# Optimization experiments

Hardware: AMD Instinct MI355X
Metric: run time of the kernel (lower is better)

Reference implementation:

```python
import jax, jax.numpy as jnp
import numpy as np

LOGISTIC_R = 3.8
COUPLING_ITERS = 5


def _linear_interp(v, L):
    """PyTorch F.interpolate(mode='linear', align_corners=False) along last axis.
    v: [..., K] real -> [..., L] real."""
    K = v.shape[-1]
    pos = (jnp.arange(L, dtype=jnp.float32) + 0.5) * (K / L) - 0.5
    pos = jnp.clip(pos, 0.0, K - 1)  # torch clamps src coords into range
    i0 = jnp.floor(pos).astype(jnp.int32)
    i1 = jnp.minimum(i0 + 1, K - 1)
    w = pos - i0
    return v[..., i0] * (1.0 - w) + v[..., i1] * w


def setup_inputs() -> dict:
    key = jax.random.key(0)
    ks = jax.random.split(key, 4)
    B, Cin, Cout, L, K = 16, 64, 64, 8192, 64
    return {
        "x_real": jax.random.normal(ks[0], (B, Cin, L), jnp.float32),
        "x_imag": jax.random.normal(ks[1], (B, Cin, L), jnp.float32),
        "kernel_real": jax.random.normal(ks[2], (Cout, Cin, K), jnp.float32),
        "kernel_imag": jax.random.normal(ks[3], (Cout, Cin, K), jnp.float32),
        "alpha_D": jnp.ones((1,), jnp.float32),
    }


def reference(x_real, x_imag, kernel_real, kernel_imag, alpha_D):
    x = x_real + 1j * x_imag  # [B, Cin, L] complex64
    L = x.shape[-1]

    # --- logistic self-coupling on magnitude (per-batch min/max over (C, L)) ---
    mag = jnp.abs(x)
    phase = jnp.angle(x)
    mmin = mag.min(axis=(-1, -2), keepdims=True)
    mmax = mag.max(axis=(-1, -2), keepdims=True)
    xn = (mag - mmin) / (mmax - mmin + 1e-10)
    for _ in range(COUPLING_ITERS):
        xn = LOGISTIC_R * xn * (1.0 - xn)
    mag_c = xn * (mmax - mmin) + mmin
    x_coupled = mag_c * jnp.exp(1j * phase)

    # --- spectral conv: FFT, per-pair kernel interpolation, complex MAC ---
    x_fft = jnp.fft.fft(x_coupled, axis=-1)  # [B, Cin, L]
    kfft = jnp.fft.fft(kernel_real + 1j * kernel_imag, axis=-1)  # [O, I, K]
    kmag = _linear_interp(jnp.abs(kfft), L)    # [O, I, L]
    kph = _linear_interp(jnp.angle(kfft), L)   # [O, I, L]
    kint = kmag * jnp.exp(1j * kph)            # [O, I, L] complex64
    out_fft = jnp.einsum('bjl,ijl->bil', x_fft, kint)  # replaces O*I python loop
    out = jnp.fft.ifft(out_fft, axis=-1)  # [B, O, L]

    # --- optical probe activation: sin(omega*0 + phi0 + alpha_D * lambda) ---
    theta = alpha_D[0] * jnp.arange(L, dtype=jnp.float32)
    act = jnp.sin(theta)  # omega*t = 0, phi0 = 0
    return out * act
```

## Files before the change

### kernel.cpp

```cpp
#include <hip/hip_runtime.h>
#include <hip/hip_fp16.h>
#include <hip/hip_bf16.h>
#include <math.h>

#define L 8192
#define LOG2L 13
#define B 16
#define CIN 64
#define COUT 64
#define KK 64

#define PI_F 3.14159265358979323846f

typedef float f4v __attribute__((ext_vector_type(4)));
typedef short s8v __attribute__((ext_vector_type(8)));

__device__ __forceinline__ int PHI(int n) { return n ^ ((((n >> 5) ^ (n >> 9)) & 15) << 1); }

__device__ __forceinline__ void nsincos(float ang, float* sn, float* cs) {
    float r = ang * 0.15915494309189535f;
    r = r - floorf(r);
    *sn = __builtin_amdgcn_sinf(r);
    *cs = __builtin_amdgcn_cosf(r);
}

__device__ __forceinline__ unsigned short f2bf(float f) {
    unsigned u = __builtin_bit_cast(unsigned, f);
    u += 0x7FFFu + ((u >> 16) & 1u);
    return (unsigned short)(u >> 16);
}
__device__ __forceinline__ unsigned pkbf(float a, float b) {
    unsigned ua = __builtin_bit_cast(unsigned, a) + 0x8000u;
    unsigned ub = __builtin_bit_cast(unsigned, b) + 0x8000u;
    return (ub & 0xFFFF0000u) | (ua >> 16);
}

template<int INV>
__device__ __forceinline__ void bfly4(float& u0r, float& u0i, float& u1r, float& u1i,
                                      float& v0r, float& v0i, float& v1r, float& v1i,
                                      float w1r, float w1i, float w2r, float w2i) {
    float A0r = u0r + v0r, A0i = u0i + v0i;
    float t0r = u0r - v0r, t0i = u0i - v0i;
    float B0r = t0r * w1r - t0i * w1i, B0i = t0r * w1i + t0i * w1r;
    float A1r = u1r + v1r, A1i = u1i + v1i;
    float t1r = u1r - v1r, t1i = u1i - v1i;
    float wr = t1r * w1r - t1i * w1i, wi = t1r * w1i + t1i * w1r;
    float B1r = INV ? -wi : wi;
    float B1i = INV ? wr : -wr;
    u0r = A0r + A1r; u0i = A0i + A1i;
    float d0r = A0r - A1r, d0i = A0i - A1i;
    u1r = d0r * w2r - d0i * w2i; u1i = d0r * w2i + d0i * w2r;
    v0r = B0r + B1r; v0i = B0i + B1i;
    float d1r = B0r - B1r, d1i = B0i - B1i;
    v1r = d1r * w2r - d1i * w2i; v1i = d1r * w2i + d1i * w2r;
}

template<int INV>
__device__ __forceinline__ void radix16(float* xr, float* xi, float wc, float ws) {
    const float C8 = 0.9238795325112867f, S8 = 0.3826834323650898f, C4 = 0.7071067811865476f;
    float e1r = C8, e1i = INV ? S8 : -S8;
    float e2r = C4, e2i = INV ? C4 : -C4;
    float e3r = S8, e3i = INV ? C8 : -C8;
    float a1r[4], a1i[4], a2r[4], a2i[4];
    a1r[0] = wc;                    a1i[0] = ws;
    a1r[1] = wc * e1r - ws * e1i;   a1i[1] = wc * e1i + ws * e1r;
    a1r[2] = wc * e2r - ws * e2i;   a1i[2] = wc * e2i + ws * e2r;
    a1r[3] = wc * e3r - ws * e3i;   a1i[3] = wc * e3i + ws * e3r;
#pragma unroll
    for (int q = 0; q < 4; ++q) {
        a2r[q] = a1r[q] * a1r[q] - a1i[q] * a1i[q];
        a2i[q] = 2.f * a1r[q] * a1i[q];
    }
    float b1r = a2r[0] * a2r[0] - a2i[0] * a2i[0], b1i = 2.f * a2r[0] * a2i[0];
    float b2r = b1r * b1r - b1i * b1i, b2i = 2.f * b1r * b1i;
#pragma unroll
    for (int q = 0; q < 4; ++q)
        bfly4<INV>(xr[q], xi[q], xr[q + 4], xi[q + 4], xr[q + 8], xi[q + 8],
                   xr[q + 12], xi[q + 12], a1r[q], a1i[q], a2r[q], a2i[q]);
#pragma unroll
    for (int c = 0; c < 4; ++c)
        bfly4<INV>(xr[4 * c], xi[4 * c], xr[4 * c + 1], xi[4 * c + 1],
                   xr[4 * c + 2], xi[4 * c + 2], xr[4 * c + 3], xi[4 * c + 3],
                   b1r, b1i, b2r, b2i);
}

__global__ __launch_bounds__(256) void k_reduce1(const float* __restrict__ xr,
                                                 const float* __restrict__ xi,
                                                 float* __restrict__ pmin,
                                                 float* __restrict__ pmax) {
    int bid = blockIdx.x;
    int batch = bid >> 6, slice = bid & 63;
    size_t base = (size_t)batch * CIN * L + (size_t)slice * L;
    int tid = threadIdx.x;
    float mn = 3.4e38f, mx = 0.0f;
    for (int r = 0; r < 32; ++r) {
        int idx = r * 256 + tid;
        float a = xr[base + idx], b = xi[base + idx];
        float m = sqrtf(a * a + b * b);
        mn = fminf(mn, m);
        mx = fmaxf(mx, m);
    }
    __shared__ float smn[4], smx[4];
    for (int off = 32; off >= 1; off >>= 1) {
        mn = fminf(mn, __shfl_down(mn, off));
        mx = fmaxf(mx, __shfl_down(mx, off));
    }
    int wave = tid >> 6;
    if ((tid & 63) == 0) { smn[wave] = mn; smx[wave] = mx; }
    __syncthreads();
    if (tid == 0) {
        for (int w = 1; w < 4; ++w) { mn = fminf(mn, smn[w]); mx = fmaxf(mx, smx[w]); }
        pmin[bid] = mn;
        pmax[bid] = mx;
    }
}

__global__ __launch_bounds__(64) void k_reduce2(const float* __restrict__ pmin,
                                                const float* __restrict__ pmax,
                                                float* __restrict__ mmin,
                                                float* __restrict__ mmax) {
    int b = blockIdx.x, t = threadIdx.x;
    float mn = pmin[b * 64 + t], mx = pmax[b * 64 + t];
    for (int off = 32; off >= 1; off >>= 1) {
        mn = fminf(mn, __shfl_down(mn, off));
        mx = fmaxf(mx, __shfl_down(mx, off));
    }
    if (t == 0) { mmin[b] = mn; mmax[b] = mx; }
}

__global__ __launch_bounds__(64) void k_kstats(const float* __restrict__ kr,
                                               const float* __restrict__ ki,
                                               float* __restrict__ Pmag,
                                               float* __restrict__ Pph) {
    int row = blockIdx.x;
    int k = threadIdx.x;
    __shared__ float sr[64], si[64];
    sr[k] = kr[row * 64 + k];
    si[k] = ki[row * 64 + k];
    __syncthreads();
    float ar = 0.f, ai = 0.f;
    for (int n = 0; n < 64; ++n) {
        int m = (n * k) & 63;
        float ang = -2.0f * PI_F * (float)m * (1.0f / 64.0f);
        float s, c;
        __sincosf(ang, &s, &c);
        ar += sr[n] * c - si[n] * s;
        ai += sr[n] * s + si[n] * c;
    }
    float mag = sqrtf(ar * ar + ai * ai);
    float ph = atan2f(ai, ar);
    int io = row >> 6, jn = row & 63;
    int ic = io >> 4, l15 = io & 15;
    int jc = jn >> 5, hi = (jn >> 3) & 3, e = jn & 7;
    int lane = hi * 16 + l15;
    size_t off = (size_t)k * 4096 + (ic * 2 + jc) * 512 + lane * 8 + e;
    Pmag[off] = mag;
    Pph[off] = ph;
    if (k == 63) {
        Pmag[off + 4096] = mag;
        Pph[off + 4096] = ph;
    }
}

__global__ __launch_bounds__(512) void k_fwd(const float* __restrict__ xr,
                                             const float* __restrict__ xi,
                                             const float* __restrict__ mmin_,
                                             const float* __restrict__ mmax_,
                                             unsigned* __restrict__ Xd) {
    __shared__ float sRe[L];
    __shared__ float sIm[L];
    int row = blockIdx.x;
    int b = row >> 6;
    int tid = threadIdx.x;
    float mmin = mmin_[b], mmax = mmax_[b];
    float span = mmax - mmin;
    float invden = 1.0f / (span + 1e-10f);
    size_t base = (size_t)row * L;

    float vr[16], vi[16];
#pragma unroll
    for (int r = 0; r < 16; ++r) {
        int idx = r * 512 + tid;
        float a = xr[base + idx], c = xi[base + idx];
        float m = sqrtf(a * a + c * c);
        float xn = (m - mmin) * invden;
#pragma unroll
        for (int it = 0; it < 5; ++it) xn = 3.8f * xn * (1.0f - xn);
        float mc = xn * span + mmin;
        float scale = (m > 0.0f) ? (mc / m) : 0.0f;
        vr[r] = a * scale;
        vi[r] = c * scale;
    }
#pragma unroll
    for (int r = 0; r < 8; ++r) {
        float sn, cs;
        nsincos(-PI_F * (float)(r * 512 + tid) * (1.0f / 4096.0f), &sn, &cs);
        float ar = vr[r], ai = vi[r], br = vr[r + 8], bi = vi[r + 8];
        vr[r] = ar + br; vi[r] = ai + bi;
        float dr = ar - br, di = ai - bi;
        vr[r + 8] = dr * cs - di * sn;
        vi[r + 8] = dr * sn + di * cs;
    }
#pragma unroll
    for (int r = 0; r < 16; ++r) {
        int a = PHI(r * 512 + tid);
        sRe[a] = vr[r]; sIm[a] = vi[r];
    }
    __syncthreads();

    {
        int j1 = tid & 255, bA = (tid >> 8) << 12;
#pragma unroll
        for (int m = 0; m < 16; ++m) {
            int a = PHI(bA + j1 + (m << 8));
            vr[m] = sRe[a]; vi[m] = sIm[a];
        }
        float sn, cs;
        nsincos(-PI_F * (float)j1 * (1.0f / 2048.0f), &sn, &cs);
        radix16<0>(vr, vi, cs, sn);
#pragma unroll
        for (int m = 0; m < 16; ++m) {
            int a = PHI(bA + j1 + (m << 8));
            sRe[a] = vr[m]; sIm[a] = vi[m];
        }
    }
    __syncthreads();
    {
        int j1 = tid & 15, bB = (tid >> 4) << 8;
#pragma unroll
        for (int m = 0; m < 16; ++m) {
            int a = PHI(bB + j1 + (m << 4));
            vr[m] = sRe[a]; vi[m] = sIm[a];
        }
        float sn, cs;
        nsincos(-PI_F * (float)j1 * (1.0f / 128.0f), &sn, &cs);
        radix16<0>(vr, vi, cs, sn);
#pragma unroll
        for (int m = 0; m < 16; ++m) {
            int a = PHI(bB + j1 + (m << 4));
            sRe[a] = vr[m]; sIm[a] = vi[m];
        }
    }
    __syncthreads();
    {
        float2* f2R = (float2*)sRe;
        float2* f2I = (float2*)sIm;
#pragma unroll
        for (int m = 0; m < 8; ++m) {
            int a = PHI(tid * 16 + 2 * m) >> 1;
            float2 vR = f2R[a], vI = f2I[a];
            vr[2 * m] = vR.x; vr[2 * m + 1] = vR.y;
            vi[2 * m] = vI.x; vi[2 * m + 1] = vI.y;
        }
        radix16<0>(vr, vi, 1.0f, 0.0f);
#pragma unroll
        for (int m = 0; m < 8; ++m) {
            int a = PHI(tid * 16 + 2 * m) >> 1;
            f2R[a] = make_float2(vr[2 * m], vr[2 * m + 1]);
            f2I[a] = make_float2(vi[2 * m], vi[2 * m + 1]);
        }
    }
    __syncthreads();

    {
        int rt = (int)(__brev((unsigned)tid) >> 23);
        unsigned o16[16];
#pragma unroll
        for (int r = 0; r < 16; ++r) {
            int a = PHI(r * 512 + rt);
            int pi = (int)(__brev((unsigned)r) >> 28);
            o16[pi] = ((unsigned)f2bf(sIm[a]) << 16) | f2bf(sRe[a]);
        }
        size_t ob = (size_t)tid * 16384 + (size_t)row * 16;
#pragma unroll
        for (int k = 0; k < 4; ++k)
            *(uint4*)&Xd[ob + 4 * k] = make_uint4(o16[4 * k], o16[4 * k + 1],
                                                  o16[4 * k + 2], o16[4 * k + 3]);
    }
}

#define PBG 8
#define REG 4624
__global__ __launch_bounds__(256) void k_gemm(const unsigned* __restrict__ X,
                                              const float* __restrict__ Pmag,
                                              const float* __restrict__ Pph,
                                              unsigned* __restrict__ outd) {
    __shared__ uint4 ldsbuf[(PBG * REG) / 16];
    char* lds = (char*)ldsbuf;
    int tid = threadIdx.x;
    int bid = blockIdx.x;
    int pwin = ((bid & 7) << 7) + (bid >> 3);
    int p0 = pwin * PBG;
    int half = pwin & 1;
    const unsigned* src = X + (size_t)(pwin >> 1) * 16384 + half * 8;

#pragma unroll
    for (int k = 0; k < 8; ++k) {
        int u = k * 256 + tid;
        int row = u >> 1;
        int g = u & 1;
        uint4 v = *(const uint4*)&src[(size_t)row * 16 + g * 4];
        int base = (row >> 6) * 144 + (row & 63) * 2;
        unsigned dw[4] = {v.x, v.y, v.z, v.w};
#pragma unroll
        for (int c = 0; c < 4; ++c) {
            int pl = g * 4 + c;
            *(unsigned short*)&lds[pl * REG + base] = (unsigned short)(dw[c] & 0xFFFFu);
            *(unsigned short*)&lds[pl * REG + 2304 + base] = (unsigned short)(dw[c] >> 16);
        }
    }
    __syncthreads();

    int lane = tid & 63, wid = tid >> 6;
    int l15 = lane & 15, l4 = lane >> 4;

    int pA = p0 + wid * 2;
    float posA = ((float)pA + 0.5f) * (1.0f / 128.0f) - 0.5f;
    posA = fmaxf(posA, 0.0f);
    int i0k = (int)posA;
    bool clampv = (i0k >= KK - 1);
    float wq[2];
#pragma unroll
    for (int q = 0; q < 2; ++q) {
        float pos = ((float)(pA + q) + 0.5f) * (1.0f / 128.0f) - 0.5f;
        pos = fmaxf(pos, 0.0f);
        wq[q] = clampv ? 0.0f : (pos - (float)i0k);
    }
    const float* mb0 = Pmag + (size_t)i0k * 4096;
    const float* pb0 = Pph + (size_t)i0k * 4096;

    f4v accR[2][4], accI[2][4];
#pragma unroll
    for (int q = 0; q < 2; ++q)
#pragma unroll
        for (int ic = 0; ic < 4; ++ic) { accR[q][ic] = (f4v)0.0f; accI[q][ic] = (f4v)0.0f; }

#pragma unroll
    for (int jc = 0; jc < 2; ++jc) {
        int jb2 = (jc * 32 + l4 * 8) * 2;
        s8v xR0 = *(const s8v*)&lds[(wid * 2 + 0) * REG + l15 * 144 + jb2];
        s8v xI0 = *(const s8v*)&lds[(wid * 2 + 0) * REG + 2304 + l15 * 144 + jb2];
        s8v xR1 = *(const s8v*)&lds[(wid * 2 + 1) * REG + l15 * 144 + jb2];
        s8v xI1 = *(const s8v*)&lds[(wid * 2 + 1) * REG + 2304 + l15 * 144 + jb2];
#pragma unroll
        for (int ic = 0; ic < 4; ++ic) {
            int tb = (ic * 2 + jc) * 512 + lane * 8;
            float4 m0a = *(const float4*)(mb0 + tb);
            float4 m0b = *(const float4*)(mb0 + tb + 4);
            float4 m1a = *(const float4*)(mb0 + 4096 + tb);
            float4 m1b = *(const float4*)(mb0 + 4096 + tb + 4);
            float4 q0a = *(const float4*)(pb0 + tb);
            float4 q0b = *(const float4*)(pb0 + tb + 4);
            float4 q1a = *(const float4*)(pb0 + 4096 + tb);
            float4 q1b = *(const float4*)(pb0 + 4096 + tb + 4);
            float m0v[8] = {m0a.x, m0a.y, m0a.z, m0a.w, m0b.x, m0b.y, m0b.z, m0b.w};
            float m1v[8] = {m1a.x, m1a.y, m1a.z, m1a.w, m1b.x, m1b.y, m1b.z, m1b.w};
            float q0v[8] = {q0a.x, q0a.y, q0a.z, q0a.w, q0b.x, q0b.y, q0b.z, q0b.w};
            float q1v[8] = {q1a.x, q1a.y, q1a.z, q1a.w, q1b.x, q1b.y, q1b.z, q1b.w};
#pragma unroll
            for (int q = 0; q < 2; ++q) {
                float w = wq[q];
                float kr[8], ki[8];
#pragma unroll
                for (int e = 0; e < 8; ++e) {
                    float mm = m0v[e] + (m1v[e] - m0v[e]) * w;
                    float ph = q0v[e] + (q1v[e] - q0v[e]) * w;
                    float sn, cs;
                    nsincos(ph, &sn, &cs);
                    kr[e] = mm * cs;
                    ki[e] = mm * sn;
                }
                union { unsigned u[4]; s8v v; } kR, kIp, kIn;
#pragma unroll
                for (int t = 0; t < 4; ++t) {
                    kR.u[t] = pkbf(kr[2 * t], kr[2 * t + 1]);
                    kIp.u[t] = pkbf(ki[2 * t], ki[2 * t + 1]);
                    kIn.u[t] = kIp.u[t] ^ 0x80008000u;
                }
                s8v xR = q ? xR1 : xR0;
                s8v xI = q ? xI1 : xI0;
                accR[q][ic] = __builtin_amdgcn_mfma_f32_16x16x32_bf16(xR, kR.v, accR[q][ic], 0, 0, 0);
                accR[q][ic] = __builtin_amdgcn_mfma_f32_16x16x32_bf16(xI, kIn.v, accR[q][ic], 0, 0, 0);
                accI[q][ic] = __builtin_amdgcn_mfma_f32_16x16x32_bf16(xR, kIp.v, accI[q][ic], 0, 0, 0);
                accI[q][ic] = __builtin_amdgcn_mfma_f32_16x16x32_bf16(xI, kR.v, accI[q][ic], 0, 0, 0);
            }
        }
    }

#pragma unroll
    for (int q = 0; q < 2; ++q) {
        int pp = wid * 2 + q;
#pragma unroll
        for (int ic = 0; ic < 4; ++ic)
#pragma unroll
            for (int e = 0; e < 4; ++e) {
                int ro = (l4 * 4 + e) * 64 + ic * 16 + l15;
                unsigned val = ((unsigned)f2bf(accI[q][ic][e]) << 16) | f2bf(accR[q][ic][e]);
                *(unsigned*)&lds[pp * REG + ro * 4] = val;
            }
    }
    __syncthreads();

#pragma unroll
    for (int k = 0; k < 32; ++k) {
        int row = k * 32 + (tid >> 3);
        unsigned v = *(const unsigned*)&lds[(tid & 7) * REG + row * 4];
        outd[(size_t)row * 8192 + p0 + (tid & 7)] = v;
    }
}

__global__ __launch_bounds__(512) void k_ifft(const __hip_bfloat162* __restrict__ outfft,
                                              const float* __restrict__ alpha_,
                                              float* __restrict__ out) {
    __shared__ float sRe[L];
    __shared__ float sIm[L];
    int row = blockIdx.x;
    int tid = threadIdx.x;
    float alpha = alpha_[0];
    size_t base = (size_t)row * L;

    float vr[16], vi[16];
#pragma unroll
    for (int r = 0; r < 16; ++r) {
        __hip_bfloat162 v = outfft[base + r * 512 + tid];
        vr[r] = __bfloat162float(v.x);
        vi[r] = __bfloat162float(v.y);
    }
#pragma unroll
    for (int r = 0; r < 8; ++r) {
        float sn, cs;
        nsincos(PI_F * (float)(r * 512 + tid) * (1.0f / 4096.0f), &sn, &cs);
        float ar = vr[r], ai = vi[r], br = vr[r + 8], bi = vi[r + 8];
        vr[r] = ar + br; vi[r] = ai + bi;
        float dr = ar - br, di = ai - bi;
        vr[r + 8] = dr * cs - di * sn;
        vi[r + 8] = dr * sn + di * cs;
    }
#pragma unroll
    for (int r = 0; r < 16; ++r) {
        int a = PHI(r * 512 + tid);
        sRe[a] = vr[r]; sIm[a] = vi[r];
    }
    __syncthreads();

    {
        int j1 = tid & 255, bA = (tid >> 8) << 12;
#pragma unroll
        for (int m = 0; m < 16; ++m) {
            int a = PHI(bA + j1 + (m << 8));
            vr[m] = sRe[a]; vi[m] = sIm[a];
        }
        float sn, cs;
        nsincos(PI_F * (float)j1 * (1.0f / 2048.0f), &sn, &cs);
        radix16<1>(vr, vi, cs, sn);
#pragma unroll
        for (int m = 0; m < 16; ++m) {
            int a = PHI(bA + j1 + (m << 8));
            sRe[a] = vr[m]; sIm[a] = vi[m];
        }
    }
    __syncthreads();
    {
        int j1 = tid & 15, bB = (tid >> 4) << 8;
#pragma unroll
        for (int m = 0; m < 16; ++m) {
            int a = PHI(bB + j1 + (m << 4));
            vr[m] = sRe[a]; vi[m] = sIm[a];
        }
        float sn, cs;
        nsincos(PI_F * (float)j1 * (1.0f / 128.0f), &sn, &cs);
        radix16<1>(vr, vi, cs, sn);
#pragma unroll
        for (int m = 0; m < 16; ++m) {
            int a = PHI(bB + j1 + (m << 4));
            sRe[a] = vr[m]; sIm[a] = vi[m];
        }
    }
    __syncthreads();
    {
        float2* f2R = (float2*)sRe;
        float2* f2I = (float2*)sIm;
#pragma unroll
        for (int m = 0; m < 8; ++m) {
            int a = PHI(tid * 16 + 2 * m) >> 1;
            float2 vR = f2R[a], vI = f2I[a];
            vr[2 * m] = vR.x; vr[2 * m + 1] = vR.y;
            vi[2 * m] = vI.x; vi[2 * m + 1] = vI.y;
        }
        radix16<1>(vr, vi, 1.0f, 0.0f);
#pragma unroll
        for (int m = 0; m < 8; ++m) {
            int a = PHI(tid * 16 + 2 * m) >> 1;
            f2R[a] = make_float2(vr[2 * m], vr[2 * m + 1]);
            f2I[a] = make_float2(vi[2 * m], vi[2 * m + 1]);
        }
    }
    __syncthreads();

    {
        int rt = (int)(__brev((unsigned)tid) >> 23);
        const float invN = 1.0f / (float)L;
        float o[16];
#pragma unroll
        for (int r = 0; r < 16; ++r) {
            int a = PHI(r * 512 + rt);
            int pi = (int)(__brev((unsigned)r) >> 28);
            int n = tid * 16 + pi;
            o[pi] = sRe[a] * sinf(alpha * (float)n) * invN;
        }
        float* dst = out + base + (size_t)tid * 16;
#pragma unroll
        for (int k = 0; k < 4; ++k)
            *(float4*)&dst[4 * k] = make_float4(o[4 * k], o[4 * k + 1],
                                                o[4 * k + 2], o[4 * k + 3]);
    }
}

extern "C" void kernel_launch(void* const* d_in, const int* in_sizes, int n_in,
                              void* d_out, int out_size, void* d_ws, size_t ws_size,
                              hipStream_t stream) {
    const float* xr = (const float*)d_in[0];
    const float* xi = (const float*)d_in[1];
    const float* kr = (const float*)d_in[2];
    const float* ki = (const float*)d_in[3];
    const float* alpha = (const float*)d_in[4];
    float* out = (float*)d_out;

    char* ws = (char*)d_ws;
    size_t OFFT_BYTES = (size_t)B * COUT * L * 4;
    size_t TBL_BYTES = (size_t)65 * 4096 * 4;
    unsigned* outfft_d = (unsigned*)ws;
    float* Pmag = (float*)(ws + OFFT_BYTES);
    float* Pph  = (float*)(ws + OFFT_BYTES + TBL_BYTES);
    float* pmin = (float*)(ws + OFFT_BYTES + 2 * TBL_BYTES);
    float* pmax = pmin + 1024;
    float* mmin = pmax + 1024;
    float* mmax = mmin + 16;

    unsigned* Xd = (unsigned*)d_out;

    hipLaunchKernelGGL(k_reduce1, dim3(1024), dim3(256), 0, stream, xr, xi, pmin, pmax);
    hipLaunchKernelGGL(k_reduce2, dim3(16), dim3(64), 0, stream, pmin, pmax, mmin, mmax);
    hipLaunchKernelGGL(k_kstats, dim3(4096), dim3(64), 0, stream, kr, ki, Pmag, Pph);
    hipLaunchKernelGGL(k_fwd, dim3(1024), dim3(512), 0, stream, xr, xi, mmin, mmax, Xd);
    hipLaunchKernelGGL(k_gemm, dim3(1024), dim3(256), 0, stream, Xd, Pmag, Pph, outfft_d);
    hipLaunchKernelGGL(k_ifft, dim3(1024), dim3(512), 0, stream,
                       (const __hip_bfloat162*)outfft_d, alpha, out);
}
```

Baseline: 130.9 us.

## Store forward FFT intermediates as packed bf16 in LDS and use twiddle recurrences

The forward FFT kernel now keeps its shared-memory scratch as packed bf16 complex words instead of two fp32 arrays. This halves LDS traffic and footprint, and the final output can be copied straight out without re-packing. Per-element sincos calls in the first radix-2 stage and in the output sin activation are replaced with rotation recurrences seeded by one sincos. sqrt and divide are replaced by rsq. The cost is extra rounding error from bf16 intermediates across the FFT stages and from accumulated recurrence drift, including the sin of large arguments for the activation.

```diff
diff --git a/kernel.cpp b/kernel.cpp
--- a/kernel.cpp
+++ b/kernel.cpp
@@ -33,6 +33,12 @@
     unsigned ua = __builtin_bit_cast(unsigned, a) + 0x8000u;
     unsigned ub = __builtin_bit_cast(unsigned, b) + 0x8000u;
     return (ub & 0xFFFF0000u) | (ua >> 16);
+}
+__device__ __forceinline__ float bf_lo(unsigned u) {
+    return __builtin_bit_cast(float, u << 16);
+}
+__device__ __forceinline__ float bf_hi(unsigned u) {
+    return __builtin_bit_cast(float, u & 0xFFFF0000u);
 }
 
 template<int INV>
@@ -167,8 +173,7 @@
                                              const float* __restrict__ mmin_,
                                              const float* __restrict__ mmax_,
                                              unsigned* __restrict__ Xd) {
-    __shared__ float sRe[L];
-    __shared__ float sIm[L];
+    __shared__ unsigned sPk[L];
     int row = blockIdx.x;
     int b = row >> 6;
     int tid = threadIdx.x;
@@ -182,82 +187,83 @@
     for (int r = 0; r < 16; ++r) {
         int idx = r * 512 + tid;
         float a = xr[base + idx], c = xi[base + idx];
-        float m = sqrtf(a * a + c * c);
+        float m2 = a * a + c * c;
+        float rinv = (m2 > 0.0f) ? __builtin_amdgcn_rsqf(m2) : 0.0f;
+        float m = m2 * rinv;
         float xn = (m - mmin) * invden;
 #pragma unroll
         for (int it = 0; it < 5; ++it) xn = 3.8f * xn * (1.0f - xn);
         float mc = xn * span + mmin;
-        float scale = (m > 0.0f) ? (mc / m) : 0.0f;
+        float scale = mc * rinv;
         vr[r] = a * scale;
         vi[r] = c * scale;
     }
-#pragma unroll
-    for (int r = 0; r < 8; ++r) {
-        float sn, cs;
-        nsincos(-PI_F * (float)(r * 512 + tid) * (1.0f / 4096.0f), &sn, &cs);
-        float ar = vr[r], ai = vi[r], br = vr[r + 8], bi = vi[r + 8];
-        vr[r] = ar + br; vi[r] = ai + bi;
-        float dr = ar - br, di = ai - bi;
-        vr[r + 8] = dr * cs - di * sn;
-        vi[r + 8] = dr * sn + di * cs;
-    }
-#pragma unroll
-    for (int r = 0; r < 16; ++r) {
-        int a = PHI(r * 512 + tid);
-        sRe[a] = vr[r]; sIm[a] = vi[r];
-    }
+    {
+        const float ER = 0.9238795325112867f, EI = -0.3826834323650898f;
+        float wr_, wi_;
+        nsincos(-PI_F * (float)tid * (1.0f / 4096.0f), &wi_, &wr_);
+#pragma unroll
+        for (int r = 0; r < 8; ++r) {
+            float ar = vr[r], ai = vi[r], br = vr[r + 8], bi = vi[r + 8];
+            vr[r] = ar + br; vi[r] = ai + bi;
+            float dr = ar - br, di = ai - bi;
+            vr[r + 8] = dr * wr_ - di * wi_;
+            vi[r + 8] = dr * wi_ + di * wr_;
+            float nr = wr_ * ER - wi_ * EI;
+            wi_ = wr_ * EI + wi_ * ER;
+            wr_ = nr;
+        }
+    }
+#pragma unroll
+    for (int r = 0; r < 16; ++r)
+        sPk[PHI(r * 512 + tid)] = pkbf(vr[r], vi[r]);
     __syncthreads();
 
     {
         int j1 = tid & 255, bA = (tid >> 8) << 12;
 #pragma unroll
         for (int m = 0; m < 16; ++m) {
-            int a = PHI(bA + j1 + (m << 8));
-            vr[m] = sRe[a]; vi[m] = sIm[a];
+            unsigned u = sPk[PHI(bA + j1 + (m << 8))];
+            vr[m] = bf_lo(u); vi[m] = bf_hi(u);
         }
         float sn, cs;
         nsincos(-PI_F * (float)j1 * (1.0f / 2048.0f), &sn, &cs);
         radix16<0>(vr, vi, cs, sn);
 #pragma unroll
+        for (int m = 0; m < 16; ++m)
+            sPk[PHI(bA + j1 + (m << 8))] = pkbf(vr[m], vi[m]);
+    }
+    __syncthreads();
+    {
+        int j1 = tid & 15, bB = (tid >> 4) << 8;
+#pragma unroll
         for (int m = 0; m < 16; ++m) {
-            int a = PHI(bA + j1 + (m << 8));
-            sRe[a] = vr[m]; sIm[a] = vi[m];
-        }
-    }
-    __syncthreads();
-    {
-        int j1 = tid & 15, bB = (tid >> 4) << 8;
-#pragma unroll
-        for (int m = 0; m < 16; ++m) {
-            int a = PHI(bB + j1 + (m << 4));
-            vr[m] = sRe[a]; vi[m] = sIm[a];
+            unsigned u = sPk[PHI(bB + j1 + (m << 4))];
+            vr[m] = bf_lo(u); vi[m] = bf_hi(u);
         }
         float sn, cs;
         nsincos(-PI_F * (float)j1 * (1.0f / 128.0f), &sn, &cs);
         radix16<0>(vr, vi, cs, sn);
 #pragma unroll
-        for (int m = 0; m < 16; ++m) {
-            int a = PHI(bB + j1 + (m << 4));
-            sRe[a] = vr[m]; sIm[a] = vi[m];
-        }
-    }
-    __syncthreads();
-    {
-        float2* f2R = (float2*)sRe;
-        float2* f2I = (float2*)sIm;
+        for (int m = 0; m < 16; ++m)
+            sPk[PHI(bB + j1 + (m << 4))] = pkbf(vr[m], vi[m]);
+    }
+    __syncthreads();
+    {
+        uint2* s2 = (uint2*)sPk;
 #pragma unroll
         for (int m = 0; m < 8; ++m) {
             int a = PHI(tid * 16 + 2 * m) >> 1;
-            float2 vR = f2R[a], vI = f2I[a];
-            vr[2 * m] = vR.x; vr[2 * m + 1] = vR.y;
-            vi[2 * m] = vI.x; vi[2 * m + 1] = vI.y;
+            uint2 u2 = s2[a];
+            vr[2 * m] = bf_lo(u2.x); vi[2 * m] = bf_hi(u2.x);
+            vr[2 * m + 1] = bf_lo(u2.y); vi[2 * m + 1] = bf_hi(u2.y);
         }
         radix16<0>(vr, vi, 1.0f, 0.0f);
 #pragma unroll
         for (int m = 0; m < 8; ++m) {
             int a = PHI(tid * 16 + 2 * m) >> 1;
-            f2R[a] = make_float2(vr[2 * m], vr[2 * m + 1]);
-            f2I[a] = make_float2(vi[2 * m], vi[2 * m + 1]);
+            s2[a] = make_uint2(pkbf(vr[2 * m], vi[2 * m]),
+                               pkbf(vr[2 * m + 1], vi[2 * m + 1]));
         }
     }
     __syncthreads();
@@ -267,9 +273,8 @@
         unsigned o16[16];
 #pragma unroll
         for (int r = 0; r < 16; ++r) {
-            int a = PHI(r * 512 + rt);
             int pi = (int)(__brev((unsigned)r) >> 28);
-            o16[pi] = ((unsigned)f2bf(sIm[a]) << 16) | f2bf(sRe[a]);
+            o16[pi] = sPk[PHI(r * 512 + rt)];
         }
         size_t ob = (size_t)tid * 16384 + (size_t)row * 16;
 #pragma unroll
@@ -426,15 +431,21 @@
         vr[r] = __bfloat162float(v.x);
         vi[r] = __bfloat162float(v.y);
     }
-#pragma unroll
-    for (int r = 0; r < 8; ++r) {
-        float sn, cs;
-        nsincos(PI_F * (float)(r * 512 + tid) * (1.0f / 4096.0f), &sn, &cs);
-        float ar = vr[r], ai = vi[r], br = vr[r + 8], bi = vi[r + 8];
-        vr[r] = ar + br; vi[r] = ai + bi;
-        float dr = ar - br, di = ai - bi;
-        vr[r + 8] = dr * cs - di * sn;
-        vi[r + 8] = dr * sn + di * cs;
+    {
+        const float ER = 0.9238795325112867f, EI = 0.3826834323650898f;
+        float wr_, wi_;
+        nsincos(PI_F * (float)tid * (1.0f / 4096.0f), &wi_, &wr_);
+#pragma unroll
+        for (int r = 0; r < 8; ++r) {
+            float ar = vr[r], ai = vi[r], br = vr[r + 8], bi = vi[r + 8];
+            vr[r] = ar + br; vi[r] = ai + bi;
+            float dr = ar - br, di = ai - bi;
+            vr[r + 8] = dr * wr_ - di * wi_;
+            vi[r + 8] = dr * wi_ + di * wr_;
+            float nr = wr_ * ER - wi_ * EI;
+            wi_ = wr_ * EI + wi_ * ER;
+            wr_ = nr;
+        }
     }
 #pragma unroll
     for (int r = 0; r < 16; ++r) {
@@ -500,13 +511,23 @@
     {
         int rt = (int)(__brev((unsigned)tid) >> 23);
         const float invN = 1.0f / (float)L;
-        float o[16];
+        float t16[16];
 #pragma unroll
         for (int r = 0; r < 16; ++r) {
             int a = PHI(r * 512 + rt);
             int pi = (int)(__brev((unsigned)r) >> 28);
-            int n = tid * 16 + pi;
-            o[pi] = sRe[a] * sinf(alpha * (float)n) * invN;
+            t16[pi] = sRe[a];
+        }
+        float sA, cA, s1, c1;
+        nsincos(alpha * (float)(tid * 16), &sA, &cA);
+        nsincos(alpha, &s1, &c1);
+        float o[16];
+#pragma unroll
+        for (int pi = 0; pi < 16; ++pi) {
+            o[pi] = t16[pi] * sA * invN;
+            float ns = sA * c1 + cA * s1;
+            cA = cA * c1 - sA * s1;
+            sA = ns;
         }
         float* dst = out + base + (size_t)tid * 16;
 #pragma unroll
```

Result: faster. 119.9 us (-8.4%).
